# Optimization experiments

Measured on AMD Instinct MI355X. Metric: run time of the kernel, lower is better.

The kernel has to match this reference:

```python
import jax, jax.numpy as jnp
import numpy as np

B, D = 32768, 1024


def setup_inputs() -> dict:
    key = jax.random.key(0)
    kx, k1, k2, k3 = jax.random.split(key, 4)
    x = jax.random.normal(kx, (B, D), dtype=jnp.float32)
    w1 = jax.random.normal(k1, (D, D), dtype=jnp.float32) * 0.1
    w2 = jax.random.normal(k2, (D, D), dtype=jnp.float32) * 0.1
    w3 = jax.random.normal(k3, (D, D), dtype=jnp.float32) * 0.1
    return {"x": x, "w1": w1, "w2": w2, "w3": w3}


def reference(x, w1, w2, w3):
    # Order 1: plain dense projection
    r1 = jnp.matmul(x, w1)  # [B, D]

    dim = x.shape[1]
    k = int(dim * 0.1)
    # Select top-k facets by mean |x| over the batch
    _, idx = jax.lax.top_k(jnp.abs(x).mean(axis=0), k)  # [k]
    mask = jnp.zeros((dim,), dtype=x.dtype).at[idx].set(1.0)  # [D]

    x_sparse = x * mask  # [B, D], zero outside active facets
    # Order 2: masked matmul, gated elementwise by the sparse input
    r2 = jnp.matmul(x_sparse, w2) * x_sparse
    # Order 3: masked matmul squared, gated elementwise
    r3 = jnp.square(jnp.matmul(x_sparse, w3)) * x_sparse
    return (r1, r2, r3)
```

## Files before the change

### kernel.cpp

```cpp
#include <hip/hip_runtime.h>
#include <hip/hip_bf16.h>
#include <stdint.h>

#define B_ROWS 32768
#define DIM    1024
#define KACT   102
#define KPAD   104
#define KP2    53

typedef short bf16x8 __attribute__((ext_vector_type(8)));
typedef unsigned short u16x8 __attribute__((ext_vector_type(8)));
typedef float f32x4  __attribute__((ext_vector_type(4)));

__device__ __forceinline__ unsigned short f2bf(float f) {
  union { float f; unsigned u; } v; v.f = f;
  unsigned u = v.u;
  unsigned r = u + 0x7fffu + ((u >> 16) & 1u);
  return (unsigned short)(r >> 16);
}
__device__ __forceinline__ float bfasf(unsigned hi16) {
  union { unsigned u; float f; } v; v.u = hi16;
  return v.f;
}

#define GLDS(g, l) __builtin_amdgcn_global_load_lds( \
    (__attribute__((address_space(1))) void*)(g),    \
    (__attribute__((address_space(3))) void*)(l), 16, 0, 0)

__global__ __launch_bounds__(256) void k_convw(
    const float* __restrict__ x, const float* __restrict__ w1,
    unsigned short* __restrict__ xb, unsigned short* __restrict__ w1t,
    float* __restrict__ partial) {
  const int t = threadIdx.x;
  if (blockIdx.x < 512) {
    const int c0 = t * 4;
    const size_t base = (size_t)blockIdx.x * 64 * DIM;
    float s0 = 0.f, s1 = 0.f, s2 = 0.f, s3 = 0.f;
    #pragma unroll 4
    for (int j = 0; j < 64; ++j) {
      size_t off = base + (size_t)j * DIM + c0;
      float4 v = *(const float4*)(x + off);
      s0 += fabsf(v.x); s1 += fabsf(v.y); s2 += fabsf(v.z); s3 += fabsf(v.w);
      ushort4 o;
      o.x = f2bf(v.x); o.y = f2bf(v.y); o.z = f2bf(v.z); o.w = f2bf(v.w);
      *(ushort4*)(xb + off) = o;
    }
    float4 p; p.x = s0; p.y = s1; p.z = s2; p.w = s3;
    *(float4*)(partial + (size_t)blockIdx.x * DIM + c0) = p;
  } else {
    __shared__ unsigned short tile[64][65];
    const int b  = blockIdx.x - 512;
    const int bx = b & 15;
    const int by = b >> 4;
    for (int e = t; e < 64 * 64; e += 256) {
      int r = e >> 6, c = e & 63;
      tile[r][c] = f2bf(w1[(size_t)(by * 64 + r) * DIM + bx * 64 + c]);
    }
    __syncthreads();
    for (int e = t; e < 64 * 64; e += 256) {
      int c = e >> 6, r = e & 63;
      w1t[(size_t)(bx * 64 + c) * DIM + by * 64 + r] = tile[r][c];
    }
  }
}

__global__ __launch_bounds__(128) void k_reduce1(const float* __restrict__ partial,
                                                 float* __restrict__ p2) {
  const int c  = (blockIdx.x & 7) * 128 + threadIdx.x;
  const int ks = blockIdx.x >> 3;
  float s = 0.f;
  #pragma unroll 8
  for (int p = ks * 64; p < ks * 64 + 64; ++p) s += partial[(size_t)p * DIM + c];
  p2[ks * DIM + c] = s;
}

__global__ __launch_bounds__(1024) void k_sel(const float* __restrict__ p2,
                                              const float* __restrict__ w2,
                                              const float* __restrict__ w3,
                                              int* __restrict__ cmap,
                                              float* __restrict__ W2sub,
                                              float* __restrict__ W3sub) {
  __shared__ double sv[DIM];
  __shared__ int wcnt[16];
  __shared__ int acts[KACT];
  const int d = threadIdx.x;
  {
    double s = 0.0;
    #pragma unroll
    for (int ks = 0; ks < 8; ++ks) s += (double)p2[ks * DIM + d];
    sv[d] = s;
  }
  __syncthreads();
  const double sd = sv[d];
  int rank = 0;
  for (int j = 0; j < DIM; ++j) {
    double s = sv[j];
    rank += (s > sd || (s == sd && j < d)) ? 1 : 0;
  }
  const int f = (rank < KACT) ? 1 : 0;
  unsigned long long m = __ballot(f != 0);
  const int lane = d & 63, w = d >> 6;
  if (lane == 0) wcnt[w] = __popcll(m);
  __syncthreads();
  int off = 0;
  for (int i = 0; i < w; ++i) off += wcnt[i];
  int pos = off + __popcll(m & ((1ull << lane) - 1ull));
  cmap[d] = f ? pos : -1;
  if (f) acts[pos] = d;
  __syncthreads();
  for (int e = d; e < KPAD * KPAD; e += 1024) {
    int i = e / KPAD, j = e - i * KPAD;
    float v2 = 0.f, v3 = 0.f;
    if (i < KACT && j < KACT) {
      size_t o = (size_t)acts[i] * DIM + acts[j];
      v2 = w2[o]; v3 = w3[o];
    }
    W2sub[e] = v2; W3sub[e] = v3;
  }
}

#define VMW4 asm volatile("s_waitcnt vmcnt(4)" ::: "memory")
#define VMW0 asm volatile("s_waitcnt vmcnt(0)" ::: "memory")
#define NOP_ (void)0

#define STAGE_A(KT) do { \
  GLDS(Abase + (size_t)sr0 * 1024 + (KT) * 32 + sc0 * 8, &Asl[((KT)&3)*8192 + p0*8]); \
  GLDS(Abase + (size_t)sr1 * 1024 + (KT) * 32 + sc1 * 8, &Asl[((KT)&3)*8192 + p1*8]); \
} while (0)
#define STAGE_B(KT) do { \
  GLDS(Bbase + (size_t)sr0 * 1024 + (KT) * 32 + sc0 * 8, &Bsl[((KT)&3)*8192 + p0*8]); \
  GLDS(Bbase + (size_t)sr1 * 1024 + (KT) * 32 + sc1 * 8, &Bsl[((KT)&3)*8192 + p1*8]); \
} while (0)

#define PH0(SLOT, STAGE_STMT) do { \
  _Pragma("unroll") for (int i = 0; i < 4; ++i) \
    areg[i] = *(const bf16x8*)(&Asl[(SLOT)*8192 + aoff0 + i * 512]); \
  _Pragma("unroll") for (int i = 0; i < 4; ++i) \
    breg[i] = *(const bf16x8*)(&Bsl[(SLOT)*8192 + boff0 + i * 512]); \
  STAGE_STMT; \
  __builtin_amdgcn_s_barrier(); \
  __builtin_amdgcn_s_setprio(1); \
  _Pragma("unroll") for (int mi = 0; mi < 4; ++mi) \
  _Pragma("unroll") for (int ni = 0; ni < 4; ++ni) \
    acc[mi][ni] = __builtin_amdgcn_mfma_f32_16x16x32_bf16(areg[mi], breg[ni], acc[mi][ni], 0, 0, 0); \
  __builtin_amdgcn_s_setprio(0); \
  __builtin_amdgcn_s_barrier(); \
} while (0)

#define PH1(SLOT, STAGE_STMT, WAIT_STMT) do { \
  _Pragma("unroll") for (int i = 0; i < 4; ++i) \
    areg[i] = *(const bf16x8*)(&Asl[(SLOT)*8192 + aoff0 + 2048 + i * 512]); \
  STAGE_STMT; \
  WAIT_STMT; \
  __builtin_amdgcn_s_barrier(); \
  __builtin_amdgcn_s_setprio(1); \
  _Pragma("unroll") for (int mi = 0; mi < 4; ++mi) \
  _Pragma("unroll") for (int ni = 0; ni < 4; ++ni) \
    acc[4 + mi][ni] = __builtin_amdgcn_mfma_f32_16x16x32_bf16(areg[mi], breg[ni], acc[4 + mi][ni], 0, 0, 0); \
  __builtin_amdgcn_s_setprio(0); \
  __builtin_amdgcn_s_barrier(); \
} while (0)

__global__ __launch_bounds__(512, 1) void k_gemm_r1(
    const unsigned short* __restrict__ A,
    const unsigned short* __restrict__ Bt,
    float* __restrict__ C) {
  __shared__ unsigned short Asl[4 * 8192];
  __shared__ unsigned short Bsl[4 * 8192];

  const int t    = threadIdx.x;
  const int lane = t & 63;
  const int wave = t >> 6;
  const int wm   = wave >> 2;
  const int wn   = wave & 3;
  const int la   = lane & 15;
  const int kg   = lane >> 4;
  const int kgx  = kg ^ ((la >> 1) & 3);

  const int swz  = (blockIdx.x & 7) * 64 + (blockIdx.x >> 3);
  const int brow = swz >> 2;
  const int bcol = swz & 3;

  const unsigned short* Abase = A  + (size_t)brow * 256 * 1024;
  const unsigned short* Bbase = Bt + (size_t)bcol * 256 * 1024;

  const int p0 = t, p1 = t + 512;
  const int q0 = p0 ^ ((p0 >> 3) & 3);
  const int q1 = p1 ^ ((p1 >> 3) & 3);
  const int sr0 = q0 >> 2, sc0 = q0 & 3;
  const int sr1 = q1 >> 2, sc1 = q1 & 3;

  const int aoff0 = (wm * 128 + la) * 32 + kgx * 8;
  const int boff0 = (wn * 64  + la) * 32 + kgx * 8;

  f32x4 acc[8][4];
  #pragma unroll
  for (int mi = 0; mi < 8; ++mi)
    #pragma unroll
    for (int ni = 0; ni < 4; ++ni)
      acc[mi][ni] = (f32x4){0.f, 0.f, 0.f, 0.f};

  bf16x8 areg[4], breg[4];

  STAGE_A(0); STAGE_B(0); STAGE_A(1); STAGE_B(1);
  VMW4;
  __builtin_amdgcn_s_barrier();

  for (int kt4 = 0; kt4 < 28; kt4 += 4) {
    PH0(0, STAGE_A(kt4 + 2)); PH1(0, STAGE_B(kt4 + 2), VMW4);
    PH0(1, STAGE_A(kt4 + 3)); PH1(1, STAGE_B(kt4 + 3), VMW4);
    PH0(2, STAGE_A(kt4 + 4)); PH1(2, STAGE_B(kt4 + 4), VMW4);
    PH0(3, STAGE_A(kt4 + 5)); PH1(3, STAGE_B(kt4 + 5), VMW4);
  }
  PH0(0, STAGE_A(30)); PH1(0, STAGE_B(30), VMW4);
  PH0(1, STAGE_A(31)); PH1(1, STAGE_B(31), VMW4);
  PH0(2, NOP_);        PH1(2, NOP_, VMW0);
  PH0(3, NOP_);        PH1(3, NOP_, NOP_);

  const int orow0 = brow * 256 + wm * 128 + (lane >> 4) * 4;
  const int ocol0 = bcol * 256 + wn * 64 + la;
  #pragma unroll
  for (int mi = 0; mi < 8; ++mi)
    #pragma unroll
    for (int ni = 0; ni < 4; ++ni)
      #pragma unroll
      for (int r = 0; r < 4; ++r)
        C[(size_t)(orow0 + mi * 16 + r) * DIM + ocol0 + ni * 16] = acc[mi][ni][r];
}

__global__ __launch_bounds__(512, 4) void k_r23(
    const unsigned short* __restrict__ xb,
    const float* __restrict__ W2sub,
    const float* __restrict__ W3sub,
    const int* __restrict__ cmap,
    float* __restrict__ out2,
    float* __restrict__ out3) {
  __shared__ unsigned int Wp2[KPAD * KP2];
  __shared__ unsigned int Wp3[KPAD * KP2];
  __shared__ float xs[2][16 * KPAD];
  __shared__ float r2s[16 * KPAD];
  __shared__ float r3s[16 * KPAD];
  __shared__ int   cms[DIM];
  const int t    = threadIdx.x;
  const int row0 = blockIdx.x * 64;

  for (int e = t; e < KPAD * 52; e += 512) {
    int i2 = e / KPAD, j = e - i2 * KPAD;
    unsigned lo2 = f2bf(W2sub[(2 * i2) * KPAD + j]);
    unsigned hi2 = f2bf(W2sub[(2 * i2 + 1) * KPAD + j]);
    Wp2[j * KP2 + i2] = lo2 | (hi2 << 16);
    unsigned lo3 = f2bf(W3sub[(2 * i2) * KPAD + j]);
    unsigned hi3 = f2bf(W3sub[(2 * i2 + 1) * KPAD + j]);
    Wp3[j * KP2 + i2] = lo3 | (hi3 << 16);
  }
  for (int e = t; e < DIM; e += 512) cms[e] = cmap[e];
  for (int e = t; e < 2 * 16 * KPAD; e += 512) ((float*)xs)[e] = 0.f;
  __syncthreads();

  const int  j   = t & 127;
  const int  rg  = (t >> 7) & 3;
  const bool jok = j < KACT;

  auto LOADR = [&](int ch, u16x8* ld) {
    const size_t base = (size_t)(row0 + ch * 16) * DIM;
    #pragma unroll
    for (int it = 0; it < 4; ++it) {
      int e = t + it * 512;
      int r = e >> 7, c8 = e & 127;
      ld[it] = *(const u16x8*)(xb + base + (size_t)r * DIM + c8 * 8);
    }
  };
  auto XSW = [&](int buf, const u16x8* ld) {
    #pragma unroll
    for (int it = 0; it < 4; ++it) {
      int e = t + it * 512;
      int r = e >> 7, c8 = e & 127;
      #pragma unroll
      for (int q = 0; q < 8; ++q) {
        int m = cms[c8 * 8 + q];
        if (m >= 0) xs[buf][r * KPAD + m] = bfasf(((unsigned)(unsigned short)ld[it][q]) << 16);
      }
    }
  };
  auto COMPUTE = [&](int buf) {
    if (jok) {
      float a2[4], a3[4];
      #pragma unroll
      for (int r = 0; r < 4; ++r) { a2[r] = 0.f; a3[r] = 0.f; }
      const unsigned int* wp2 = &Wp2[j * KP2];
      const unsigned int* wp3 = &Wp3[j * KP2];
      for (int g = 0; g < 26; ++g) {
        unsigned ua = wp2[2 * g], ub = wp2[2 * g + 1];
        unsigned va = wp3[2 * g], vb = wp3[2 * g + 1];
        float w2v0 = bfasf(ua << 16), w2v1 = bfasf(ua & 0xFFFF0000u);
        float w2v2 = bfasf(ub << 16), w2v3 = bfasf(ub & 0xFFFF0000u);
        float w3v0 = bfasf(va << 16), w3v1 = bfasf(va & 0xFFFF0000u);
        float w3v2 = bfasf(vb << 16), w3v3 = bfasf(vb & 0xFFFF0000u);
        #pragma unroll
        for (int r = 0; r < 4; ++r) {
          f32x4 xv = *(const f32x4*)(&xs[buf][(rg * 4 + r) * KPAD + g * 4]);
          a2[r] += xv[0] * w2v0 + xv[1] * w2v1 + xv[2] * w2v2 + xv[3] * w2v3;
          a3[r] += xv[0] * w3v0 + xv[1] * w3v1 + xv[2] * w3v2 + xv[3] * w3v3;
        }
      }
      #pragma unroll
      for (int r = 0; r < 4; ++r) {
        int rr = rg * 4 + r;
        float g = xs[buf][rr * KPAD + j];
        r2s[rr * KPAD + j] = a2[r] * g;
        r3s[rr * KPAD + j] = a3[r] * a3[r] * g;
      }
    }
  };
  auto WRITEOUT = [&](int ch) {
    const int r0 = row0 + ch * 16;
    const int c0 = (t & 255) * 4;
    const int rh = t >> 8;
    const int4 cm = *(const int4*)(&cms[c0]);
    #pragma unroll
    for (int k = 0; k < 8; ++k) {
      int r = rh + k * 2;
      const float* rr2 = &r2s[r * KPAD];
      const float* rr3 = &r3s[r * KPAD];
      float4 o2, o3;
      o2.x = (cm.x >= 0) ? rr2[cm.x] : 0.f;  o3.x = (cm.x >= 0) ? rr3[cm.x] : 0.f;
      o2.y = (cm.y >= 0) ? rr2[cm.y] : 0.f;  o3.y = (cm.y >= 0) ? rr3[cm.y] : 0.f;
      o2.z = (cm.z >= 0) ? rr2[cm.z] : 0.f;  o3.z = (cm.z >= 0) ? rr3[cm.z] : 0.f;
      o2.w = (cm.w >= 0) ? rr2[cm.w] : 0.f;  o3.w = (cm.w >= 0) ? rr3[cm.w] : 0.f;
      size_t oo = (size_t)(r0 + r) * DIM + c0;
      *(float4*)(out2 + oo) = o2;
      *(float4*)(out3 + oo) = o3;
    }
  };

  u16x8 ldA[4], ldB[4];
  LOADR(0, ldA);
  XSW(0, ldA);
  __syncthreads();
  LOADR(1, ldB); COMPUTE(0); __syncthreads(); WRITEOUT(0); XSW(1, ldB); __syncthreads();
  LOADR(2, ldA); COMPUTE(1); __syncthreads(); WRITEOUT(1); XSW(0, ldA); __syncthreads();
  LOADR(3, ldB); COMPUTE(0); __syncthreads(); WRITEOUT(2); XSW(1, ldB); __syncthreads();
  COMPUTE(1); __syncthreads(); WRITEOUT(3);
}

extern "C" void kernel_launch(void* const* d_in, const int* in_sizes, int n_in,
                              void* d_out, int out_size, void* d_ws, size_t ws_size,
                              hipStream_t stream) {
  const float* x  = (const float*)d_in[0];
  const float* w1 = (const float*)d_in[1];
  const float* w2 = (const float*)d_in[2];
  const float* w3 = (const float*)d_in[3];

  float* out1 = (float*)d_out;
  float* out2 = out1 + (size_t)B_ROWS * DIM;
  float* out3 = out2 + (size_t)B_ROWS * DIM;

  char* ws = (char*)d_ws;
  unsigned short* xb     = (unsigned short*)ws;
  unsigned short* w1t    = (unsigned short*)(ws + 67108864);
  float*          partial= (float*)(ws + 69206016);
  float*          p2     = (float*)(ws + 71303168);
  int*            cmap   = (int*)(ws + 71335936);
  float*          W2sub  = (float*)(ws + 71340032);
  float*          W3sub  = (float*)(ws + 71383296);

  k_convw   <<<dim3(768), dim3(256),  0, stream>>>(x, w1, xb, w1t, partial);
  k_reduce1 <<<dim3(64),  dim3(128),  0, stream>>>(partial, p2);
  k_sel     <<<dim3(1),   dim3(1024), 0, stream>>>(p2, w2, w3, cmap, W2sub, W3sub);
  k_gemm_r1 <<<dim3(512), dim3(512),  0, stream>>>(xb, w1t, out1);
  k_r23     <<<dim3(512), dim3(512),  0, stream>>>(xb, W2sub, W3sub, cmap, out2, out3);
}
```

Baseline: 267.4 us.

## Simplify GEMM pipeline, move weight gather into r23, drop double buffering

Drops the W2sub/W3sub gather from the single-block selection kernel; each r23 block now gathers the active submatrix of w2/w3 straight from global memory. The GEMM merges its two half-phases into one phase per k-step, loading 8 A fragments and issuing all 32 MFMAs at once. Its launch bounds rise to request 2 blocks per CU. The r23 kernel replaces its double-buffered prefetch with a plain sequential loop, which removes load/compute overlap but frees LDS. The higher register demand from 8 A fragments under a 2-block occupancy target risks spills, and every r23 block now repeats the scattered weight gather.

```diff
diff --git a/kernel.cpp b/kernel.cpp
--- a/kernel.cpp
+++ b/kernel.cpp
@@ -75,14 +75,10 @@
 }
 
 __global__ __launch_bounds__(1024) void k_sel(const float* __restrict__ p2,
-                                              const float* __restrict__ w2,
-                                              const float* __restrict__ w3,
-                                              int* __restrict__ cmap,
-                                              float* __restrict__ W2sub,
-                                              float* __restrict__ W3sub) {
+                                              int* __restrict__ act,
+                                              int* __restrict__ cmap) {
   __shared__ double sv[DIM];
   __shared__ int wcnt[16];
-  __shared__ int acts[KACT];
   const int d = threadIdx.x;
   {
     double s = 0.0;
@@ -106,62 +102,37 @@
   for (int i = 0; i < w; ++i) off += wcnt[i];
   int pos = off + __popcll(m & ((1ull << lane) - 1ull));
   cmap[d] = f ? pos : -1;
-  if (f) acts[pos] = d;
-  __syncthreads();
-  for (int e = d; e < KPAD * KPAD; e += 1024) {
-    int i = e / KPAD, j = e - i * KPAD;
-    float v2 = 0.f, v3 = 0.f;
-    if (i < KACT && j < KACT) {
-      size_t o = (size_t)acts[i] * DIM + acts[j];
-      v2 = w2[o]; v3 = w3[o];
-    }
-    W2sub[e] = v2; W3sub[e] = v3;
-  }
+  if (f) act[pos] = d;
 }
 
 #define VMW4 asm volatile("s_waitcnt vmcnt(4)" ::: "memory")
 #define VMW0 asm volatile("s_waitcnt vmcnt(0)" ::: "memory")
 #define NOP_ (void)0
 
-#define STAGE_A(KT) do { \
+#define STAGE(KT) do { \
   GLDS(Abase + (size_t)sr0 * 1024 + (KT) * 32 + sc0 * 8, &Asl[((KT)&3)*8192 + p0*8]); \
   GLDS(Abase + (size_t)sr1 * 1024 + (KT) * 32 + sc1 * 8, &Asl[((KT)&3)*8192 + p1*8]); \
-} while (0)
-#define STAGE_B(KT) do { \
   GLDS(Bbase + (size_t)sr0 * 1024 + (KT) * 32 + sc0 * 8, &Bsl[((KT)&3)*8192 + p0*8]); \
   GLDS(Bbase + (size_t)sr1 * 1024 + (KT) * 32 + sc1 * 8, &Bsl[((KT)&3)*8192 + p1*8]); \
 } while (0)
 
-#define PH0(SLOT, STAGE_STMT) do { \
-  _Pragma("unroll") for (int i = 0; i < 4; ++i) \
+#define PH(SLOT, STAGE_STMT, WAIT_STMT) do { \
+  _Pragma("unroll") for (int i = 0; i < 8; ++i) \
     areg[i] = *(const bf16x8*)(&Asl[(SLOT)*8192 + aoff0 + i * 512]); \
   _Pragma("unroll") for (int i = 0; i < 4; ++i) \
     breg[i] = *(const bf16x8*)(&Bsl[(SLOT)*8192 + boff0 + i * 512]); \
   STAGE_STMT; \
+  WAIT_STMT; \
   __builtin_amdgcn_s_barrier(); \
   __builtin_amdgcn_s_setprio(1); \
-  _Pragma("unroll") for (int mi = 0; mi < 4; ++mi) \
+  _Pragma("unroll") for (int mi = 0; mi < 8; ++mi) \
   _Pragma("unroll") for (int ni = 0; ni < 4; ++ni) \
     acc[mi][ni] = __builtin_amdgcn_mfma_f32_16x16x32_bf16(areg[mi], breg[ni], acc[mi][ni], 0, 0, 0); \
   __builtin_amdgcn_s_setprio(0); \
   __builtin_amdgcn_s_barrier(); \
 } while (0)
 
-#define PH1(SLOT, STAGE_STMT, WAIT_STMT) do { \
-  _Pragma("unroll") for (int i = 0; i < 4; ++i) \
-    areg[i] = *(const bf16x8*)(&Asl[(SLOT)*8192 + aoff0 + 2048 + i * 512]); \
-  STAGE_STMT; \
-  WAIT_STMT; \
-  __builtin_amdgcn_s_barrier(); \
-  __builtin_amdgcn_s_setprio(1); \
-  _Pragma("unroll") for (int mi = 0; mi < 4; ++mi) \
-  _Pragma("unroll") for (int ni = 0; ni < 4; ++ni) \
-    acc[4 + mi][ni] = __builtin_amdgcn_mfma_f32_16x16x32_bf16(areg[mi], breg[ni], acc[4 + mi][ni], 0, 0, 0); \
-  __builtin_amdgcn_s_setprio(0); \
-  __builtin_amdgcn_s_barrier(); \
-} while (0)
-
-__global__ __launch_bounds__(512, 1) void k_gemm_r1(
+__global__ __launch_bounds__(512, 2) void k_gemm_r1(
     const unsigned short* __restrict__ A,
     const unsigned short* __restrict__ Bt,
     float* __restrict__ C) {
@@ -200,22 +171,22 @@
     for (int ni = 0; ni < 4; ++ni)
       acc[mi][ni] = (f32x4){0.f, 0.f, 0.f, 0.f};
 
-  bf16x8 areg[4], breg[4];
-
-  STAGE_A(0); STAGE_B(0); STAGE_A(1); STAGE_B(1);
+  bf16x8 areg[8], breg[4];
+
+  STAGE(0); STAGE(1);
   VMW4;
   __builtin_amdgcn_s_barrier();
 
   for (int kt4 = 0; kt4 < 28; kt4 += 4) {
-    PH0(0, STAGE_A(kt4 + 2)); PH1(0, STAGE_B(kt4 + 2), VMW4);
-    PH0(1, STAGE_A(kt4 + 3)); PH1(1, STAGE_B(kt4 + 3), VMW4);
-    PH0(2, STAGE_A(kt4 + 4)); PH1(2, STAGE_B(kt4 + 4), VMW4);
-    PH0(3, STAGE_A(kt4 + 5)); PH1(3, STAGE_B(kt4 + 5), VMW4);
-  }
-  PH0(0, STAGE_A(30)); PH1(0, STAGE_B(30), VMW4);
-  PH0(1, STAGE_A(31)); PH1(1, STAGE_B(31), VMW4);
-  PH0(2, NOP_);        PH1(2, NOP_, VMW0);
-  PH0(3, NOP_);        PH1(3, NOP_, NOP_);
+    PH(0, STAGE(kt4 + 2), VMW4);
+    PH(1, STAGE(kt4 + 3), VMW4);
+    PH(2, STAGE(kt4 + 4), VMW4);
+    PH(3, STAGE(kt4 + 5), VMW4);
+  }
+  PH(0, STAGE(30), VMW4);
+  PH(1, STAGE(31), VMW4);
+  PH(2, NOP_, VMW0);
+  PH(3, NOP_, NOP_);
 
   const int orow0 = brow * 256 + wm * 128 + (lane >> 4) * 4;
   const int ocol0 = bcol * 256 + wn * 64 + la;
@@ -230,59 +201,62 @@
 
 __global__ __launch_bounds__(512, 4) void k_r23(
     const unsigned short* __restrict__ xb,
-    const float* __restrict__ W2sub,
-    const float* __restrict__ W3sub,
+    const float* __restrict__ w2,
+    const float* __restrict__ w3,
+    const int* __restrict__ act,
     const int* __restrict__ cmap,
     float* __restrict__ out2,
     float* __restrict__ out3) {
   __shared__ unsigned int Wp2[KPAD * KP2];
   __shared__ unsigned int Wp3[KPAD * KP2];
-  __shared__ float xs[2][16 * KPAD];
+  __shared__ float xs [16 * KPAD];
   __shared__ float r2s[16 * KPAD];
   __shared__ float r3s[16 * KPAD];
   __shared__ int   cms[DIM];
+  __shared__ int   acts[KACT];
   const int t    = threadIdx.x;
   const int row0 = blockIdx.x * 64;
 
+  if (t < KACT) acts[t] = act[t];
+  for (int e = t; e < DIM; e += 512) cms[e] = cmap[e];
+  if (t < 16) { xs[t * KPAD + 102] = 0.f; xs[t * KPAD + 103] = 0.f; }
+  __syncthreads();
+
   for (int e = t; e < KPAD * 52; e += 512) {
     int i2 = e / KPAD, j = e - i2 * KPAD;
-    unsigned lo2 = f2bf(W2sub[(2 * i2) * KPAD + j]);
-    unsigned hi2 = f2bf(W2sub[(2 * i2 + 1) * KPAD + j]);
-    Wp2[j * KP2 + i2] = lo2 | (hi2 << 16);
-    unsigned lo3 = f2bf(W3sub[(2 * i2) * KPAD + j]);
-    unsigned hi3 = f2bf(W3sub[(2 * i2 + 1) * KPAD + j]);
-    Wp3[j * KP2 + i2] = lo3 | (hi3 << 16);
-  }
-  for (int e = t; e < DIM; e += 512) cms[e] = cmap[e];
-  for (int e = t; e < 2 * 16 * KPAD; e += 512) ((float*)xs)[e] = 0.f;
+    float lo2 = 0.f, hi2 = 0.f, lo3 = 0.f, hi3 = 0.f;
+    if (j < KACT && i2 < 51) {
+      int cj = acts[j];
+      size_t o0 = (size_t)acts[2 * i2] * DIM + cj;
+      size_t o1 = (size_t)acts[2 * i2 + 1] * DIM + cj;
+      lo2 = w2[o0]; hi2 = w2[o1];
+      lo3 = w3[o0]; hi3 = w3[o1];
+    }
+    Wp2[j * KP2 + i2] = (unsigned)f2bf(lo2) | ((unsigned)f2bf(hi2) << 16);
+    Wp3[j * KP2 + i2] = (unsigned)f2bf(lo3) | ((unsigned)f2bf(hi3) << 16);
+  }
   __syncthreads();
 
   const int  j   = t & 127;
   const int  rg  = (t >> 7) & 3;
   const bool jok = j < KACT;
 
-  auto LOADR = [&](int ch, u16x8* ld) {
-    const size_t base = (size_t)(row0 + ch * 16) * DIM;
-    #pragma unroll
-    for (int it = 0; it < 4; ++it) {
-      int e = t + it * 512;
-      int r = e >> 7, c8 = e & 127;
-      ld[it] = *(const u16x8*)(xb + base + (size_t)r * DIM + c8 * 8);
-    }
-  };
-  auto XSW = [&](int buf, const u16x8* ld) {
-    #pragma unroll
-    for (int it = 0; it < 4; ++it) {
-      int e = t + it * 512;
-      int r = e >> 7, c8 = e & 127;
-      #pragma unroll
-      for (int q = 0; q < 8; ++q) {
-        int m = cms[c8 * 8 + q];
-        if (m >= 0) xs[buf][r * KPAD + m] = bfasf(((unsigned)(unsigned short)ld[it][q]) << 16);
+  for (int ch = 0; ch < 4; ++ch) {
+    {
+      const size_t base = (size_t)(row0 + ch * 16) * DIM;
+      #pragma unroll
+      for (int it = 0; it < 4; ++it) {
+        int e = t + it * 512;
+        int r = e >> 7, c8 = e & 127;
+        u16x8 v = *(const u16x8*)(xb + base + (size_t)r * DIM + c8 * 8);
+        #pragma unroll
+        for (int q = 0; q < 8; ++q) {
+          int m = cms[c8 * 8 + q];
+          if (m >= 0) xs[r * KPAD + m] = bfasf(((unsigned)(unsigned short)v[q]) << 16);
+        }
       }
     }
-  };
-  auto COMPUTE = [&](int buf) {
+    __syncthreads();
     if (jok) {
       float a2[4], a3[4];
       #pragma unroll
@@ -298,7 +272,7 @@
         float w3v2 = bfasf(vb << 16), w3v3 = bfasf(vb & 0xFFFF0000u);
         #pragma unroll
         for (int r = 0; r < 4; ++r) {
-          f32x4 xv = *(const f32x4*)(&xs[buf][(rg * 4 + r) * KPAD + g * 4]);
+          f32x4 xv = *(const f32x4*)(&xs[(rg * 4 + r) * KPAD + g * 4]);
           a2[r] += xv[0] * w2v0 + xv[1] * w2v1 + xv[2] * w2v2 + xv[3] * w2v3;
           a3[r] += xv[0] * w3v0 + xv[1] * w3v1 + xv[2] * w3v2 + xv[3] * w3v3;
         }
@@ -306,41 +280,34 @@
       #pragma unroll
       for (int r = 0; r < 4; ++r) {
         int rr = rg * 4 + r;
-        float g = xs[buf][rr * KPAD + j];
+        float g = xs[rr * KPAD + j];
         r2s[rr * KPAD + j] = a2[r] * g;
         r3s[rr * KPAD + j] = a3[r] * a3[r] * g;
       }
     }
-  };
-  auto WRITEOUT = [&](int ch) {
-    const int r0 = row0 + ch * 16;
-    const int c0 = (t & 255) * 4;
-    const int rh = t >> 8;
-    const int4 cm = *(const int4*)(&cms[c0]);
-    #pragma unroll
-    for (int k = 0; k < 8; ++k) {
-      int r = rh + k * 2;
-      const float* rr2 = &r2s[r * KPAD];
-      const float* rr3 = &r3s[r * KPAD];
-      float4 o2, o3;
-      o2.x = (cm.x >= 0) ? rr2[cm.x] : 0.f;  o3.x = (cm.x >= 0) ? rr3[cm.x] : 0.f;
-      o2.y = (cm.y >= 0) ? rr2[cm.y] : 0.f;  o3.y = (cm.y >= 0) ? rr3[cm.y] : 0.f;
-      o2.z = (cm.z >= 0) ? rr2[cm.z] : 0.f;  o3.z = (cm.z >= 0) ? rr3[cm.z] : 0.f;
-      o2.w = (cm.w >= 0) ? rr2[cm.w] : 0.f;  o3.w = (cm.w >= 0) ? rr3[cm.w] : 0.f;
-      size_t oo = (size_t)(r0 + r) * DIM + c0;
-      *(float4*)(out2 + oo) = o2;
-      *(float4*)(out3 + oo) = o3;
-    }
-  };
-
-  u16x8 ldA[4], ldB[4];
-  LOADR(0, ldA);
-  XSW(0, ldA);
-  __syncthreads();
-  LOADR(1, ldB); COMPUTE(0); __syncthreads(); WRITEOUT(0); XSW(1, ldB); __syncthreads();
-  LOADR(2, ldA); COMPUTE(1); __syncthreads(); WRITEOUT(1); XSW(0, ldA); __syncthreads();
-  LOADR(3, ldB); COMPUTE(0); __syncthreads(); WRITEOUT(2); XSW(1, ldB); __syncthreads();
-  COMPUTE(1); __syncthreads(); WRITEOUT(3);
+    __syncthreads();
+    {
+      const int r0 = row0 + ch * 16;
+      const int c0 = (t & 255) * 4;
+      const int rh = t >> 8;
+      const int4 cm = *(const int4*)(&cms[c0]);
+      #pragma unroll
+      for (int k = 0; k < 8; ++k) {
+        int r = rh + k * 2;
+        const float* rr2 = &r2s[r * KPAD];
+        const float* rr3 = &r3s[r * KPAD];
+        float4 o2, o3;
+        o2.x = (cm.x >= 0) ? rr2[cm.x] : 0.f;  o3.x = (cm.x >= 0) ? rr3[cm.x] : 0.f;
+        o2.y = (cm.y >= 0) ? rr2[cm.y] : 0.f;  o3.y = (cm.y >= 0) ? rr3[cm.y] : 0.f;
+        o2.z = (cm.z >= 0) ? rr2[cm.z] : 0.f;  o3.z = (cm.z >= 0) ? rr3[cm.z] : 0.f;
+        o2.w = (cm.w >= 0) ? rr2[cm.w] : 0.f;  o3.w = (cm.w >= 0) ? rr3[cm.w] : 0.f;
+        size_t oo = (size_t)(r0 + r) * DIM + c0;
+        *(float4*)(out2 + oo) = o2;
+        *(float4*)(out3 + oo) = o3;
+      }
+    }
+    __syncthreads();
+  }
 }
 
 extern "C" void kernel_launch(void* const* d_in, const int* in_sizes, int n_in,
@@ -361,12 +328,11 @@
   float*          partial= (float*)(ws + 69206016);
   float*          p2     = (float*)(ws + 71303168);
   int*            cmap   = (int*)(ws + 71335936);
-  float*          W2sub  = (float*)(ws + 71340032);
-  float*          W3sub  = (float*)(ws + 71383296);
+  int*            act    = (int*)(ws + 71340032);
 
   k_convw   <<<dim3(768), dim3(256),  0, stream>>>(x, w1, xb, w1t, partial);
   k_reduce1 <<<dim3(64),  dim3(128),  0, stream>>>(partial, p2);
-  k_sel     <<<dim3(1),   dim3(1024), 0, stream>>>(p2, w2, w3, cmap, W2sub, W3sub);
+  k_sel     <<<dim3(1),   dim3(1024), 0, stream>>>(p2, act, cmap);
   k_gemm_r1 <<<dim3(512), dim3(512),  0, stream>>>(xb, w1t, out1);
-  k_r23     <<<dim3(512), dim3(512),  0, stream>>>(xb, W2sub, W3sub, cmap, out2, out3);
-}
+  k_r23     <<<dim3(512), dim3(512),  0, stream>>>(xb, w2, w3, act, cmap, out2, out3);
+}
```

Result: slower. 276.5 us (+3.4%).
